# Optimization experiments

Measured on AMD Instinct MI355X. Metric: run time of the kernel, lower is better.

Reference implementation:

```python
import jax, jax.numpy as jnp
import numpy as np

B, S, IN = 16, 512, 32
D, H, L = 768, 12, 6
DH = D // H
DFF = 4 * D
EPS = 1e-5
NEG = -1e9


def _ln(x, g, b):
    m = jnp.mean(x, axis=-1, keepdims=True)
    v = jnp.mean(jnp.square(x - m), axis=-1, keepdims=True)
    return (x - m) * jax.lax.rsqrt(v + EPS) * g + b


def setup_inputs() -> dict:
    key = jax.random.key(0)
    ks = jax.random.split(key, 24)
    nrm = lambda k, shape, s=0.02: jax.random.normal(k, shape, jnp.float32) * s
    inp = {
        'x': jax.random.normal(ks[0], (B, S, IN), jnp.float32),
        'event_lengths': jax.random.randint(ks[1], (B,), 1, S + 1),
        'in_w': nrm(ks[2], (IN, D)),
        'in_b': jnp.zeros((D,), jnp.float32),
        'pos_emb': nrm(ks[3], (S, D)),
        'qw': nrm(ks[4], (L, D, D)), 'qb': jnp.zeros((L, D), jnp.float32),
        'kw': nrm(ks[5], (L, D, D)), 'kb': jnp.zeros((L, D), jnp.float32),
        'vw': nrm(ks[6], (L, D, D)), 'vb': jnp.zeros((L, D), jnp.float32),
        'w1': nrm(ks[7], (L, D, DFF)), 'b1': jnp.zeros((L, DFF), jnp.float32),
        'w2': nrm(ks[8], (L, DFF, D)), 'b2': jnp.zeros((L, D), jnp.float32),
        'ln1_g': jnp.ones((L, D), jnp.float32), 'ln1_b': jnp.zeros((L, D), jnp.float32),
        'ln2_g': jnp.ones((L, D), jnp.float32), 'ln2_b': jnp.zeros((L, D), jnp.float32),
        'out_w': nrm(ks[9], (D, 1)), 'out_b': jnp.zeros((1,), jnp.float32),
    }
    return inp


def reference(x, event_lengths, in_w, in_b, pos_emb, qw, qb, kw, kb, vw, vb,
              w1, b1, w2, b2, ln1_g, ln1_b, ln2_g, ln2_b, out_w, out_b):
    b, s, _ = x.shape
    h = x @ in_w + in_b + pos_emb[None, :s]  # [B,S,D]
    valid = jnp.arange(s)[None, :] < event_lengths[:, None]  # [B,S]
    amask = valid[:, None, :, None] & valid[:, None, None, :]  # [B,1,S,S]
    scale = np.float32(1.0 / np.sqrt(DH))
    for l in range(qw.shape[0]):
        q = (h @ qw[l] + qb[l]).reshape(b, s, H, DH)
        k = (h @ kw[l] + kb[l]).reshape(b, s, H, DH)
        v = (h @ vw[l] + vb[l]).reshape(b, s, H, DH)
        scores = jnp.einsum('bqhd,bkhd->bhqk', q, k) * scale
        scores = jnp.where(amask, scores, NEG)
        p = jax.nn.softmax(scores, axis=-1)
        o = jnp.einsum('bhqk,bkhd->bqhd', p, v).reshape(b, s, -1)
        # NOTE: source overwrites summarize(...) output with the raw concat, so no out-proj
        h = _ln(h + o, ln1_g[l], ln1_b[l])
        ff = jnp.maximum(h @ w1[l] + b1[l], 0.0) @ w2[l] + b2[l]
        h = _ln(h + ff, ln2_g[l], ln2_b[l])
    pooled = jnp.where(valid[..., None], h, 0.0).sum(axis=1) / event_lengths[:, None].astype(h.dtype)
    return pooled @ out_w + out_b  # [B,1]
```

## Files before the change

kernel.cpp:

```cpp
#include <hip/hip_runtime.h>

typedef unsigned short u16;
typedef unsigned int u32;
typedef u16 u16x8 __attribute__((ext_vector_type(8)));
typedef u16 u16x4 __attribute__((ext_vector_type(4)));
typedef __bf16 bf16x8 __attribute__((ext_vector_type(8)));
typedef float f32x4 __attribute__((ext_vector_type(4)));

#define DEV __device__ __forceinline__

DEV u16 f2bf(float f) {
  u32 u = __builtin_bit_cast(u32, f);
  u32 r = u + 0x7fffu + ((u >> 16) & 1u);
  return (u16)(r >> 16);
}

DEV int imin(int a, int b) { return a < b ? a : b; }

DEV void gload_lds16(const void* g, void* l) {
  __builtin_amdgcn_global_load_lds(
      (const __attribute__((address_space(1))) void*)g,
      (__attribute__((address_space(3))) void*)l, 16, 0, 0);
}

template <int RELU, int OUT_BF16>
__global__ __launch_bounds__(256, 3) void gemm97_kernel(
    const u16* __restrict__ A, const u16* __restrict__ Bt,
    const float* __restrict__ bias, u16* __restrict__ Cb, float* __restrict__ Cf,
    int M, int N, int ksub, int ld, int nsplit) {
  __shared__ __align__(16) u16 As[128 * 64];
  __shared__ __align__(16) u16 Bs[128 * 64];
  const int t = threadIdx.x, wave = t >> 6, lane = t & 63;
  const int fr = lane & 15, fq = lane >> 4;
  const int NT = ksub >> 6;
  const int nbx = N >> 7;
  const int tiles = nbx * (M >> 7);

  int bid = blockIdx.x;
  {
    const int cpx = (int)gridDim.x >> 3;
    bid = (bid & 7) * cpx + (bid >> 3);
  }
  const int sp = bid / tiles;
  bid -= sp * tiles;
  const int bx = bid % nbx, by = bid / nbx;
  const int m0 = by << 7, n0 = bx << 7;

  const int srow = t >> 3;
  const int c8 = ((t & 7) ^ (srow & 7)) * 8;
  const u16* ag = A + (size_t)sp * ksub + (size_t)(m0 + srow) * ld + c8;
  const u16* bg = Bt + (size_t)sp * ksub + (size_t)(n0 + srow) * ld + c8;
  char* asb = (char*)As + wave * 1024;
  char* bsb = (char*)Bs + wave * 1024;

  const int wr = (wave >> 1) * 64, wc = (wave & 1) * 64;
  f32x4 acc[4][4] = {};

  for (int k0 = 0; k0 < NT; ++k0) {
#pragma unroll
    for (int i = 0; i < 4; ++i) {
      gload_lds16(ag + (size_t)i * 32 * ld, asb + i * 4096);
      gload_lds16(bg + (size_t)i * 32 * ld, bsb + i * 4096);
    }
    ag += 64;
    bg += 64;
    asm volatile("s_waitcnt vmcnt(0)" ::: "memory");
    __syncthreads();
#pragma unroll
    for (int ks = 0; ks < 2; ++ks) {
      bf16x8 af[4], bv[4];
#pragma unroll
      for (int m = 0; m < 4; ++m)
        af[m] = *(const bf16x8*)(As + (wr + m * 16 + fr) * 64 + (((ks * 4 + fq) ^ (fr & 7)) * 8));
#pragma unroll
      for (int n = 0; n < 4; ++n)
        bv[n] = *(const bf16x8*)(Bs + (wc + n * 16 + fr) * 64 + (((ks * 4 + fq) ^ (fr & 7)) * 8));
#pragma unroll
      for (int m = 0; m < 4; ++m)
#pragma unroll
        for (int n = 0; n < 4; ++n)
          acc[m][n] = __builtin_amdgcn_mfma_f32_16x16x32_bf16(af[m], bv[n], acc[m][n], 0, 0, 0);
    }
    __syncthreads();
  }

#pragma unroll
  for (int n = 0; n < 4; ++n) {
    const int col = n0 + wc + n * 16 + fr;
    const float bvv = (nsplit == 1 || sp == 0) ? bias[col] : 0.f;
#pragma unroll
    for (int m = 0; m < 4; ++m) {
#pragma unroll
      for (int r = 0; r < 4; ++r) {
        const int row = m0 + wr + m * 16 + fq * 4 + r;
        float v = acc[m][n][r] + bvv;
        if (RELU) v = fmaxf(v, 0.f);
        if (OUT_BF16)
          Cb[(size_t)row * N + col] = f2bf(v);
        else
          Cf[(size_t)sp * M * N + (size_t)row * N + col] = v;
      }
    }
  }
}

__global__ __launch_bounds__(256, 2) void attn_kernel(const u16* __restrict__ qkv,
                                                      const int* __restrict__ lens,
                                                      float* __restrict__ o) {
  __shared__ __align__(16) u16 Kl[128 * 64];
  __shared__ __align__(16) u16 Vt[64 * 128];
  __shared__ __align__(16) u16 Pl[4][16 * 128];

  const int bid = blockIdx.x;
  const int qt = bid & 7;
  const int h = (bid >> 3) % 12;
  const int b = bid / 96;
  const int len = lens[b];
  const int t = threadIdx.x, wave = t >> 6, lane = t & 63;
  const int fr = lane & 15, fq = lane >> 4;

  const size_t base = (size_t)b * 512 * 2304;
  const int q0 = qt * 64 + wave * 16;

  bf16x8 qf[2];
#pragma unroll
  for (int ks = 0; ks < 2; ++ks)
    qf[ks] = *(const bf16x8*)(qkv + base + (size_t)(q0 + fr) * 2304 + h * 64 + ks * 32 + fq * 8);

  f32x4 oacc[4] = {};
  float mrow[4], lrow[4];
#pragma unroll
  for (int r = 0; r < 4; ++r) {
    mrow[r] = -1e30f;
    lrow[r] = 0.f;
  }

  for (int kv0 = 0; kv0 < 512; kv0 += 128) {
    if (kv0 >= len) break;
#pragma unroll
    for (int i = 0; i < 4; ++i) {
      const int c = i * 256 + t;
      const int row = c >> 3, ch = c & 7;
      u16x8 kvl = *(const u16x8*)(qkv + base + (size_t)(kv0 + row) * 2304 + 768 + h * 64 + ch * 8);
      *(u16x8*)(Kl + row * 64 + ((ch ^ (row & 7)) * 8)) = kvl;
      u16x8 vvl = *(const u16x8*)(qkv + base + (size_t)(kv0 + row) * 2304 + 1536 + h * 64 + ch * 8);
#pragma unroll
      for (int u = 0; u < 8; ++u) {
        const int d = ch * 8 + u;
        Vt[d * 128 + (((row >> 3) ^ (d & 7)) * 8) + (row & 7)] = vvl[u];
      }
    }
    __syncthreads();

    f32x4 sa[8] = {};
#pragma unroll
    for (int ks = 0; ks < 2; ++ks) {
#pragma unroll
      for (int n = 0; n < 8; ++n) {
        const int colr = n * 16 + fr;
        bf16x8 kf = *(const bf16x8*)(Kl + colr * 64 + (((ks * 4 + fq) ^ (colr & 7)) * 8));
        sa[n] = __builtin_amdgcn_mfma_f32_16x16x32_bf16(qf[ks], kf, sa[n], 0, 0, 0);
      }
    }

    float tm[4] = {-1e30f, -1e30f, -1e30f, -1e30f};
#pragma unroll
    for (int n = 0; n < 8; ++n) {
      const int col = kv0 + n * 16 + fr;
      const bool ok = col < len;
#pragma unroll
      for (int r = 0; r < 4; ++r) {
        const float s = ok ? sa[n][r] * 0.125f : -1e30f;
        sa[n][r] = s;
        tm[r] = fmaxf(tm[r], s);
      }
    }
#pragma unroll
    for (int d = 1; d < 16; d <<= 1)
#pragma unroll
      for (int r = 0; r < 4; ++r) tm[r] = fmaxf(tm[r], __shfl_xor(tm[r], d));

    float al[4], rs[4];
#pragma unroll
    for (int r = 0; r < 4; ++r) {
      const float mn = fmaxf(mrow[r], tm[r]);
      al[r] = __expf(mrow[r] - mn);
      mrow[r] = mn;
      rs[r] = 0.f;
    }
#pragma unroll
    for (int n = 0; n < 8; ++n)
#pragma unroll
      for (int r = 0; r < 4; ++r) {
        const float p = __expf(sa[n][r] - mrow[r]);
        sa[n][r] = p;
        rs[r] += p;
      }
#pragma unroll
    for (int d = 1; d < 16; d <<= 1)
#pragma unroll
      for (int r = 0; r < 4; ++r) rs[r] += __shfl_xor(rs[r], d);
#pragma unroll
    for (int r = 0; r < 4; ++r) lrow[r] = lrow[r] * al[r] + rs[r];
#pragma unroll
    for (int n = 0; n < 4; ++n)
#pragma unroll
      for (int r = 0; r < 4; ++r) oacc[n][r] *= al[r];

    u16* P = &Pl[wave][0];
#pragma unroll
    for (int n = 0; n < 8; ++n) {
      const int col = n * 16 + fr;
#pragma unroll
      for (int r = 0; r < 4; ++r) {
        const int row = fq * 4 + r;
        P[row * 128 + (((col >> 3) ^ (row & 7)) * 8) + (col & 7)] = f2bf(sa[n][r]);
      }
    }
#pragma unroll
    for (int kslot = 0; kslot < 4; ++kslot) {
      const int ch = kslot * 4 + fq;
      bf16x8 pa = *(const bf16x8*)(P + fr * 128 + ((ch ^ (fr & 7)) * 8));
#pragma unroll
      for (int n = 0; n < 4; ++n) {
        const int colv = n * 16 + fr;
        bf16x8 vf = *(const bf16x8*)(Vt + colv * 128 + ((ch ^ (colv & 7)) * 8));
        oacc[n] = __builtin_amdgcn_mfma_f32_16x16x32_bf16(pa, vf, oacc[n], 0, 0, 0);
      }
    }
    __syncthreads();
  }

  const size_t obase = (size_t)b * 512 * 768 + (size_t)q0 * 768 + h * 64;
#pragma unroll
  for (int n = 0; n < 4; ++n)
#pragma unroll
    for (int r = 0; r < 4; ++r)
      o[obase + (size_t)(fq * 4 + r) * 768 + n * 16 + fr] = oacc[n][r] / lrow[r];
}

__global__ __launch_bounds__(256) void transpose_all_kernel(
    const float* __restrict__ qw, const float* __restrict__ kw, const float* __restrict__ vw,
    const float* __restrict__ w1, const float* __restrict__ w2, u16* __restrict__ qkvt6,
    u16* __restrict__ w1t6, u16* __restrict__ w2t6) {
  __shared__ float tile[64][65];
  const int l = blockIdx.y;
  int x = blockIdx.x;
  const float* in;
  u16* op;
  int K, N, nbx;
  if (x < 432) {
    const int which = x / 144;
    x -= which * 144;
    in = (which == 0 ? qw : which == 1 ? kw : vw) + (size_t)l * 768 * 768;
    op = qkvt6 + (size_t)l * 2304 * 768 + (size_t)which * 768 * 768;
    K = 768;
    N = 768;
    nbx = 12;
  } else if (x < 1008) {
    x -= 432;
    in = w1 + (size_t)l * 768 * 3072;
    op = w1t6 + (size_t)l * 3072 * 768;
    K = 768;
    N = 3072;
    nbx = 48;
  } else {
    x -= 1008;
    in = w2 + (size_t)l * 3072 * 768;
    op = w2t6 + (size_t)l * 768 * 3072;
    K = 3072;
    N = 768;
    nbx = 12;
  }
  const int tx = threadIdx.x & 63, ty = threadIdx.x >> 6;
  const int n0 = (x % nbx) * 64, k0 = (x / nbx) * 64;
#pragma unroll
  for (int i = 0; i < 16; ++i)
    tile[ty + i * 4][tx] = in[(size_t)(k0 + ty + i * 4) * N + n0 + tx];
  __syncthreads();
#pragma unroll
  for (int i = 0; i < 16; ++i)
    op[(size_t)(n0 + ty + i * 4) * K + k0 + tx] = f2bf(tile[tx][ty + i * 4]);
}

__global__ __launch_bounds__(256) void inproj_kernel(const float* __restrict__ x,
                                                     const float* __restrict__ in_w,
                                                     const float* __restrict__ in_b,
                                                     const float* __restrict__ pos,
                                                     float* __restrict__ h,
                                                     u16* __restrict__ hbf) {
  __shared__ float xs[8][32];
  const int t = threadIdx.x;
  const int row0 = blockIdx.x * 8;
  xs[t >> 5][t & 31] = x[(size_t)row0 * 32 + t];
  __syncthreads();
#pragma unroll
  for (int j = 0; j < 3; ++j) {
    const int d = t + j * 256;
    float acc[8] = {};
#pragma unroll
    for (int i = 0; i < 32; ++i) {
      const float wv = in_w[i * 768 + d];
#pragma unroll
      for (int r = 0; r < 8; ++r) acc[r] += xs[r][i] * wv;
    }
    const float bb = in_b[d];
#pragma unroll
    for (int r = 0; r < 8; ++r) {
      const int row = row0 + r;
      const int s = row & 511;
      const float v = acc[r] + bb + pos[(size_t)s * 768 + d];
      h[(size_t)row * 768 + d] = v;
      hbf[(size_t)row * 768 + d] = f2bf(v);
    }
  }
}

template <int ND>
__global__ __launch_bounds__(256) void ln_kernel(const float* __restrict__ hin,
                                                 const float* __restrict__ d0,
                                                 const float* __restrict__ d1,
                                                 const float* __restrict__ g,
                                                 const float* __restrict__ bb,
                                                 float* __restrict__ hout,
                                                 u16* __restrict__ hbf) {
  const int row = blockIdx.x * 4 + (threadIdx.x >> 6);
  const int lane = threadIdx.x & 63;
  const size_t rb = (size_t)row * 768 + lane * 4;
  f32x4 xv[3];
  float s = 0.f, s2 = 0.f;
#pragma unroll
  for (int j = 0; j < 3; ++j) {
    f32x4 a = *(const f32x4*)(hin + rb + j * 256);
    f32x4 d = *(const f32x4*)(d0 + rb + j * 256);
    f32x4 v = a + d;
    if (ND == 2) {
      f32x4 e = *(const f32x4*)(d1 + rb + j * 256);
      v = v + e;
    }
    xv[j] = v;
    s += v[0] + v[1] + v[2] + v[3];
    s2 += v[0] * v[0] + v[1] * v[1] + v[2] * v[2] + v[3] * v[3];
  }
#pragma unroll
  for (int d = 1; d < 64; d <<= 1) {
    s += __shfl_xor(s, d);
    s2 += __shfl_xor(s2, d);
  }
  const float mean = s * (1.f / 768.f);
  const float var = fmaxf(s2 * (1.f / 768.f) - mean * mean, 0.f);
  const float rstd = rsqrtf(var + 1e-5f);
#pragma unroll
  for (int j = 0; j < 3; ++j) {
    f32x4 gv = *(const f32x4*)(g + lane * 4 + j * 256);
    f32x4 bv = *(const f32x4*)(bb + lane * 4 + j * 256);
    f32x4 y;
    u16x4 yb;
#pragma unroll
    for (int c = 0; c < 4; ++c) {
      y[c] = (xv[j][c] - mean) * rstd * gv[c] + bv[c];
      yb[c] = f2bf(y[c]);
    }
    *(f32x4*)(hout + rb + j * 256) = y;
    *(u16x4*)(hbf + rb + j * 256) = yb;
  }
}

__global__ __launch_bounds__(256) void pool1_kernel(const float* __restrict__ h,
                                                    const int* __restrict__ lens,
                                                    const float* __restrict__ ow,
                                                    float* __restrict__ wsp) {
  const int b = blockIdx.x >> 3, chunk = blockIdx.x & 7;
  const int len = lens[b];
  const int t = threadIdx.x;
  const int s0 = chunk * 64;
  const int s1 = imin(s0 + 64, len);
  float acc0 = 0.f, acc1 = 0.f, acc2 = 0.f;
  const float* hp = h + (size_t)b * 512 * 768;
  for (int s = s0; s < s1; ++s) {
    const size_t rb = (size_t)s * 768;
    acc0 += hp[rb + t];
    acc1 += hp[rb + t + 256];
    acc2 += hp[rb + t + 512];
  }
  float part = acc0 * ow[t] + acc1 * ow[t + 256] + acc2 * ow[t + 512];
#pragma unroll
  for (int d = 1; d < 64; d <<= 1) part += __shfl_xor(part, d);
  __shared__ float ps[4];
  if ((t & 63) == 0) ps[t >> 6] = part;
  __syncthreads();
  if (t == 0) wsp[blockIdx.x] = ps[0] + ps[1] + ps[2] + ps[3];
}

__global__ void pool2_kernel(const float* __restrict__ wsp, const int* __restrict__ lens,
                             const float* __restrict__ ob, float* __restrict__ out) {
  const int b = threadIdx.x;
  if (b < 16) {
    float s = 0.f;
#pragma unroll
    for (int c = 0; c < 8; ++c) s += wsp[b * 8 + c];
    out[b] = s / (float)lens[b] + ob[0];
  }
}

__global__ void biaspack_kernel(const float* __restrict__ qb, const float* __restrict__ kb,
                                const float* __restrict__ vb, float* __restrict__ qkvb) {
  const int i = blockIdx.x * 256 + threadIdx.x;
  if (i >= 6 * 2304) return;
  const int l = i / 2304, j = i % 2304;
  float v;
  if (j < 768)
    v = qb[l * 768 + j];
  else if (j < 1536)
    v = kb[l * 768 + j - 768];
  else
    v = vb[l * 768 + j - 1536];
  qkvb[i] = v;
}

extern "C" void kernel_launch(void* const* d_in, const int* in_sizes, int n_in, void* d_out,
                              int out_size, void* d_ws, size_t ws_size, hipStream_t stream) {
  const float* x = (const float*)d_in[0];
  const int* lens = (const int*)d_in[1];
  const float* in_w = (const float*)d_in[2];
  const float* in_b = (const float*)d_in[3];
  const float* pos = (const float*)d_in[4];
  const float* qw = (const float*)d_in[5];
  const float* qb = (const float*)d_in[6];
  const float* kw = (const float*)d_in[7];
  const float* kb = (const float*)d_in[8];
  const float* vw = (const float*)d_in[9];
  const float* vb = (const float*)d_in[10];
  const float* w1 = (const float*)d_in[11];
  const float* b1 = (const float*)d_in[12];
  const float* w2 = (const float*)d_in[13];
  const float* b2 = (const float*)d_in[14];
  const float* ln1g = (const float*)d_in[15];
  const float* ln1b = (const float*)d_in[16];
  const float* ln2g = (const float*)d_in[17];
  const float* ln2b = (const float*)d_in[18];
  const float* ow = (const float*)d_in[19];
  const float* ob = (const float*)d_in[20];
  float* out = (float*)d_out;

  char* w = (char*)d_ws;
  size_t off = 0;
  auto alloc = [&](size_t bytes) -> void* {
    void* p = w + off;
    off += (bytes + 255) & ~(size_t)255;
    return p;
  };
  u16* qkvt6 = (u16*)alloc((size_t)6 * 2304 * 768 * 2);
  u16* w1t6 = (u16*)alloc((size_t)6 * 3072 * 768 * 2);
  u16* w2t6 = (u16*)alloc((size_t)6 * 768 * 3072 * 2);
  float* qkvb = (float*)alloc((size_t)6 * 2304 * 4);
  float* h = (float*)alloc((size_t)8192 * 768 * 4);
  u16* hbf = (u16*)alloc((size_t)8192 * 768 * 2);
  float* obuf = (float*)alloc((size_t)2 * 8192 * 768 * 4);
  u16* ubuf = (u16*)alloc((size_t)8192 * 3072 * 2);
  float* wsp = (float*)alloc((size_t)128 * 4);
  u16* qkvbuf = ubuf;
  u16* ffbuf = ubuf;

  biaspack_kernel<<<(6 * 2304 + 255) / 256, 256, 0, stream>>>(qb, kb, vb, qkvb);
  transpose_all_kernel<<<dim3(1584, 6), 256, 0, stream>>>(qw, kw, vw, w1, w2, qkvt6, w1t6, w2t6);
  inproj_kernel<<<1024, 256, 0, stream>>>(x, in_w, in_b, pos, h, hbf);

  for (int l = 0; l < 6; ++l) {
    gemm97_kernel<0, 1><<<1152, 256, 0, stream>>>(hbf, qkvt6 + (size_t)l * 2304 * 768,
                                                  qkvb + l * 2304, qkvbuf, nullptr, 8192, 2304,
                                                  768, 768, 1);
    attn_kernel<<<1536, 256, 0, stream>>>(qkvbuf, lens, obuf);
    ln_kernel<1><<<2048, 256, 0, stream>>>(h, obuf, nullptr, ln1g + l * 768, ln1b + l * 768, h,
                                           hbf);
    gemm97_kernel<1, 1><<<1536, 256, 0, stream>>>(hbf, w1t6 + (size_t)l * 3072 * 768,
                                                  b1 + l * 3072, ffbuf, nullptr, 8192, 3072, 768,
                                                  768, 1);
    gemm97_kernel<0, 0><<<768, 256, 0, stream>>>(ffbuf, w2t6 + (size_t)l * 768 * 3072,
                                                 b2 + l * 768, nullptr, obuf, 8192, 768, 1536,
                                                 3072, 2);
    ln_kernel<2><<<2048, 256, 0, stream>>>(h, obuf, obuf + (size_t)8192 * 768, ln2g + l * 768,
                                           ln2b + l * 768, h, hbf);
  }
  pool1_kernel<<<128, 256, 0, stream>>>(h, lens, ow, wsp);
  pool2_kernel<<<1, 64, 0, stream>>>(wsp, lens, ob, out);
  (void)in_sizes;
  (void)n_in;
  (void)out_size;
  (void)ws_size;
}
```

Before: 1.427 ms.

## Use bf16 intermediates, drop FF2 split-K, skip padded attention query tiles

```diff
diff --git a/kernel.cpp b/kernel.cpp
--- a/kernel.cpp
+++ b/kernel.cpp
@@ -15,6 +15,8 @@
   return (u16)(r >> 16);
 }
 
+DEV float bf2f(u16 v) { return __builtin_bit_cast(float, (u32)v << 16); }
+
 DEV int imin(int a, int b) { return a < b ? a : b; }
 
 DEV void gload_lds16(const void* g, void* l) {
@@ -23,33 +25,29 @@
       (__attribute__((address_space(3))) void*)l, 16, 0, 0);
 }
 
-template <int RELU, int OUT_BF16>
+template <int RELU>
 __global__ __launch_bounds__(256, 3) void gemm97_kernel(
     const u16* __restrict__ A, const u16* __restrict__ Bt,
-    const float* __restrict__ bias, u16* __restrict__ Cb, float* __restrict__ Cf,
-    int M, int N, int ksub, int ld, int nsplit) {
+    const float* __restrict__ bias, u16* __restrict__ Cb, int M, int N, int K) {
   __shared__ __align__(16) u16 As[128 * 64];
   __shared__ __align__(16) u16 Bs[128 * 64];
   const int t = threadIdx.x, wave = t >> 6, lane = t & 63;
   const int fr = lane & 15, fq = lane >> 4;
-  const int NT = ksub >> 6;
+  const int NT = K >> 6;
   const int nbx = N >> 7;
-  const int tiles = nbx * (M >> 7);
 
   int bid = blockIdx.x;
   {
     const int cpx = (int)gridDim.x >> 3;
     bid = (bid & 7) * cpx + (bid >> 3);
   }
-  const int sp = bid / tiles;
-  bid -= sp * tiles;
   const int bx = bid % nbx, by = bid / nbx;
   const int m0 = by << 7, n0 = bx << 7;
 
   const int srow = t >> 3;
   const int c8 = ((t & 7) ^ (srow & 7)) * 8;
-  const u16* ag = A + (size_t)sp * ksub + (size_t)(m0 + srow) * ld + c8;
-  const u16* bg = Bt + (size_t)sp * ksub + (size_t)(n0 + srow) * ld + c8;
+  const u16* ag = A + (size_t)(m0 + srow) * K + c8;
+  const u16* bg = Bt + (size_t)(n0 + srow) * K + c8;
   char* asb = (char*)As + wave * 1024;
   char* bsb = (char*)Bs + wave * 1024;
 
@@ -59,8 +57,8 @@
   for (int k0 = 0; k0 < NT; ++k0) {
 #pragma unroll
     for (int i = 0; i < 4; ++i) {
-      gload_lds16(ag + (size_t)i * 32 * ld, asb + i * 4096);
-      gload_lds16(bg + (size_t)i * 32 * ld, bsb + i * 4096);
+      gload_lds16(ag + (size_t)i * 32 * K, asb + i * 4096);
+      gload_lds16(bg + (size_t)i * 32 * K, bsb + i * 4096);
     }
     ag += 64;
     bg += 64;
@@ -87,7 +85,7 @@
 #pragma unroll
   for (int n = 0; n < 4; ++n) {
     const int col = n0 + wc + n * 16 + fr;
-    const float bvv = (nsplit == 1 || sp == 0) ? bias[col] : 0.f;
+    const float bvv = bias[col];
 #pragma unroll
     for (int m = 0; m < 4; ++m) {
 #pragma unroll
@@ -95,10 +93,7 @@
         const int row = m0 + wr + m * 16 + fq * 4 + r;
         float v = acc[m][n][r] + bvv;
         if (RELU) v = fmaxf(v, 0.f);
-        if (OUT_BF16)
-          Cb[(size_t)row * N + col] = f2bf(v);
-        else
-          Cf[(size_t)sp * M * N + (size_t)row * N + col] = v;
+        Cb[(size_t)row * N + col] = f2bf(v);
       }
     }
   }
@@ -106,7 +101,7 @@
 
 __global__ __launch_bounds__(256, 2) void attn_kernel(const u16* __restrict__ qkv,
                                                       const int* __restrict__ lens,
-                                                      float* __restrict__ o) {
+                                                      u16* __restrict__ o) {
   __shared__ __align__(16) u16 Kl[128 * 64];
   __shared__ __align__(16) u16 Vt[64 * 128];
   __shared__ __align__(16) u16 Pl[4][16 * 128];
@@ -116,6 +111,7 @@
   const int h = (bid >> 3) % 12;
   const int b = bid / 96;
   const int len = lens[b];
+  if (qt * 64 >= len) return;
   const int t = threadIdx.x, wave = t >> 6, lane = t & 63;
   const int fr = lane & 15, fq = lane >> 4;
 
@@ -236,51 +232,57 @@
   for (int n = 0; n < 4; ++n)
 #pragma unroll
     for (int r = 0; r < 4; ++r)
-      o[obase + (size_t)(fq * 4 + r) * 768 + n * 16 + fr] = oacc[n][r] / lrow[r];
+      o[obase + (size_t)(fq * 4 + r) * 768 + n * 16 + fr] = f2bf(oacc[n][r] / lrow[r]);
 }
 
 __global__ __launch_bounds__(256) void transpose_all_kernel(
     const float* __restrict__ qw, const float* __restrict__ kw, const float* __restrict__ vw,
     const float* __restrict__ w1, const float* __restrict__ w2, u16* __restrict__ qkvt6,
     u16* __restrict__ w1t6, u16* __restrict__ w2t6) {
-  __shared__ float tile[64][65];
+  __shared__ u16 tile[128 * 65];
   const int l = blockIdx.y;
   int x = blockIdx.x;
   const float* in;
   u16* op;
   int K, N, nbx;
-  if (x < 432) {
-    const int which = x / 144;
-    x -= which * 144;
+  if (x < 216) {
+    const int which = x / 72;
+    x -= which * 72;
     in = (which == 0 ? qw : which == 1 ? kw : vw) + (size_t)l * 768 * 768;
     op = qkvt6 + (size_t)l * 2304 * 768 + (size_t)which * 768 * 768;
     K = 768;
     N = 768;
     nbx = 12;
-  } else if (x < 1008) {
-    x -= 432;
+  } else if (x < 504) {
+    x -= 216;
     in = w1 + (size_t)l * 768 * 3072;
     op = w1t6 + (size_t)l * 3072 * 768;
     K = 768;
     N = 3072;
     nbx = 48;
   } else {
-    x -= 1008;
+    x -= 504;
     in = w2 + (size_t)l * 3072 * 768;
     op = w2t6 + (size_t)l * 768 * 3072;
     K = 3072;
     N = 768;
     nbx = 12;
   }
+  const int n0 = (x % nbx) * 64, k0 = (x / nbx) * 128;
   const int tx = threadIdx.x & 63, ty = threadIdx.x >> 6;
-  const int n0 = (x % nbx) * 64, k0 = (x / nbx) * 64;
-#pragma unroll
-  for (int i = 0; i < 16; ++i)
-    tile[ty + i * 4][tx] = in[(size_t)(k0 + ty + i * 4) * N + n0 + tx];
+#pragma unroll
+  for (int i = 0; i < 32; ++i) {
+    const int kr = ty + i * 4;
+    tile[kr * 65 + tx] = f2bf(in[(size_t)(k0 + kr) * N + n0 + tx]);
+  }
   __syncthreads();
 #pragma unroll
-  for (int i = 0; i < 16; ++i)
-    op[(size_t)(n0 + ty + i * 4) * K + k0 + tx] = f2bf(tile[tx][ty + i * 4]);
+  for (int i = 0; i < 16; ++i) {
+    const int nr = ty + i * 4;
+    const u32 lo = tile[(2 * tx) * 65 + nr];
+    const u32 hi = tile[(2 * tx + 1) * 65 + nr];
+    *(u32*)(op + (size_t)(n0 + nr) * K + k0 + 2 * tx) = lo | (hi << 16);
+  }
 }
 
 __global__ __launch_bounds__(256) void inproj_kernel(const float* __restrict__ x,
@@ -316,10 +318,8 @@
   }
 }
 
-template <int ND>
 __global__ __launch_bounds__(256) void ln_kernel(const float* __restrict__ hin,
-                                                 const float* __restrict__ d0,
-                                                 const float* __restrict__ d1,
+                                                 const u16* __restrict__ delta,
                                                  const float* __restrict__ g,
                                                  const float* __restrict__ bb,
                                                  float* __restrict__ hout,
@@ -332,12 +332,10 @@
 #pragma unroll
   for (int j = 0; j < 3; ++j) {
     f32x4 a = *(const f32x4*)(hin + rb + j * 256);
-    f32x4 d = *(const f32x4*)(d0 + rb + j * 256);
-    f32x4 v = a + d;
-    if (ND == 2) {
-      f32x4 e = *(const f32x4*)(d1 + rb + j * 256);
-      v = v + e;
-    }
+    u16x4 dv = *(const u16x4*)(delta + rb + j * 256);
+    f32x4 v;
+#pragma unroll
+    for (int c = 0; c < 4; ++c) v[c] = a[c] + bf2f(dv[c]);
     xv[j] = v;
     s += v[0] + v[1] + v[2] + v[3];
     s2 += v[0] * v[0] + v[1] * v[1] + v[2] * v[2] + v[3] * v[3];
@@ -456,31 +454,26 @@
   float* qkvb = (float*)alloc((size_t)6 * 2304 * 4);
   float* h = (float*)alloc((size_t)8192 * 768 * 4);
   u16* hbf = (u16*)alloc((size_t)8192 * 768 * 2);
-  float* obuf = (float*)alloc((size_t)2 * 8192 * 768 * 4);
+  u16* obuf = (u16*)alloc((size_t)8192 * 768 * 2);
   u16* ubuf = (u16*)alloc((size_t)8192 * 3072 * 2);
   float* wsp = (float*)alloc((size_t)128 * 4);
   u16* qkvbuf = ubuf;
   u16* ffbuf = ubuf;
 
   biaspack_kernel<<<(6 * 2304 + 255) / 256, 256, 0, stream>>>(qb, kb, vb, qkvb);
-  transpose_all_kernel<<<dim3(1584, 6), 256, 0, stream>>>(qw, kw, vw, w1, w2, qkvt6, w1t6, w2t6);
+  transpose_all_kernel<<<dim3(792, 6), 256, 0, stream>>>(qw, kw, vw, w1, w2, qkvt6, w1t6, w2t6);
   inproj_kernel<<<1024, 256, 0, stream>>>(x, in_w, in_b, pos, h, hbf);
 
   for (int l = 0; l < 6; ++l) {
-    gemm97_kernel<0, 1><<<1152, 256, 0, stream>>>(hbf, qkvt6 + (size_t)l * 2304 * 768,
-                                                  qkvb + l * 2304, qkvbuf, nullptr, 8192, 2304,
-                                                  768, 768, 1);
+    gemm97_kernel<0><<<1152, 256, 0, stream>>>(hbf, qkvt6 + (size_t)l * 2304 * 768,
+                                               qkvb + l * 2304, qkvbuf, 8192, 2304, 768);
     attn_kernel<<<1536, 256, 0, stream>>>(qkvbuf, lens, obuf);
-    ln_kernel<1><<<2048, 256, 0, stream>>>(h, obuf, nullptr, ln1g + l * 768, ln1b + l * 768, h,
-                                           hbf);
-    gemm97_kernel<1, 1><<<1536, 256, 0, stream>>>(hbf, w1t6 + (size_t)l * 3072 * 768,
-                                                  b1 + l * 3072, ffbuf, nullptr, 8192, 3072, 768,
-                                                  768, 1);
-    gemm97_kernel<0, 0><<<768, 256, 0, stream>>>(ffbuf, w2t6 + (size_t)l * 768 * 3072,
-                                                 b2 + l * 768, nullptr, obuf, 8192, 768, 1536,
-                                                 3072, 2);
-    ln_kernel<2><<<2048, 256, 0, stream>>>(h, obuf, obuf + (size_t)8192 * 768, ln2g + l * 768,
-                                           ln2b + l * 768, h, hbf);
+    ln_kernel<<<2048, 256, 0, stream>>>(h, obuf, ln1g + l * 768, ln1b + l * 768, h, hbf);
+    gemm97_kernel<1><<<1536, 256, 0, stream>>>(hbf, w1t6 + (size_t)l * 3072 * 768, b1 + l * 3072,
+                                               ffbuf, 8192, 3072, 768);
+    gemm97_kernel<0><<<384, 256, 0, stream>>>(ffbuf, w2t6 + (size_t)l * 768 * 3072, b2 + l * 768,
+                                              obuf, 8192, 768, 3072);
+    ln_kernel<<<2048, 256, 0, stream>>>(h, obuf, ln2g + l * 768, ln2b + l * 768, h, hbf);
   }
   pool1_kernel<<<128, 256, 0, stream>>>(h, lens, ow, wsp);
   pool2_kernel<<<1, 64, 0, stream>>>(wsp, lens, ob, out);
```

Measured after the change: 1.492 ms. 1.05x slower.
